# Kernel optimization log

Measured on AMD Instinct MI355X. Metric: run time of the kernel, lower is better.

Reference implementation:

```python
import jax, jax.numpy as jnp
import numpy as np

TEMP = 0.1
LAM = 1.0
NORM_EPS = 1e-12   # torch F.normalize eps
COS_EPS = 1e-8     # torch F.cosine_similarity eps


def l2norm(x, axis):
    n = jnp.sqrt(jnp.sum(x * x, axis=axis, keepdims=True))
    return x / jnp.maximum(n, NORM_EPS)


def cos_sim(a, b, axis):
    na = jnp.sqrt(jnp.sum(a * a, axis=axis))
    nb = jnp.sqrt(jnp.sum(b * b, axis=axis))
    return jnp.sum(a * b, axis=axis) / jnp.maximum(na * nb, COS_EPS)


def setup_inputs() -> dict:
    key = jax.random.key(0)
    k1, k2, k3, k4, k5 = jax.random.split(key, 5)
    B, C, H, W = 32, 256, 32, 32
    return {
        "q_b": jax.random.normal(k1, (B, C, H, W), dtype=jnp.float32),
        "k_b": jax.random.normal(k2, (B, C, H, W), dtype=jnp.float32),
        "q_grid": jax.random.normal(k3, (B, C, H, W), dtype=jnp.float32),
        "k_grid": jax.random.normal(k4, (B, C, H, W), dtype=jnp.float32),
        "labels": jax.random.randint(k5, (B,), 0, 10, dtype=jnp.int64),
    }


def densecl(q_b, k_b, q_grid, k_grid, labels):
    B, C, H, W = q_b.shape
    S = H * W
    q_b = l2norm(q_b, axis=1)
    k_b = l2norm(k_b, axis=1)
    q_grid = l2norm(q_grid, axis=1)
    k_grid = l2norm(k_grid, axis=1)

    q_b_flat = q_b.reshape(B, C, S)
    k_b_flat = k_b.reshape(B, C, S)
    # spatial correspondence: [B, S, S]
    sim = jnp.einsum('bci,bcj->bij', q_b_flat, k_b_flat)
    max_sim_idx = jnp.argmax(sim, axis=-1)  # [B, S]

    Cg = q_grid.shape[1]
    q_grid_flat = q_grid.reshape(B, Cg, S)
    k_grid_flat = k_grid.reshape(B, Cg, S)
    idx = jnp.broadcast_to(max_sim_idx[:, None, :], (B, Cg, S))
    k_matched = jnp.take_along_axis(k_grid_flat, idx, axis=2)
    pos_sim = cos_sim(q_grid_flat, k_matched, axis=1) / TEMP  # [B, S]

    # random negative from a different-label sample (use_prototypes=False path)
    key = jax.random.key(42)
    u = jax.random.uniform(key, (B, B))
    mask = labels[:, None] != labels[None, :]
    neg_idx = jnp.argmax(jnp.where(mask, u, -1.0), axis=1)  # [B]
    neg_k = k_grid_flat[neg_idx]  # [B, Cg, S]
    neg_sim = cos_sim(q_grid_flat, neg_k, axis=1) / TEMP  # [B, S]

    loss = -jnp.log(jnp.exp(pos_sim) / (jnp.exp(pos_sim) + jnp.exp(neg_sim) + 1e-6))
    return jnp.mean(loss)


def reference(q_b, k_b, q_grid, k_grid, labels):
    return densecl(q_b, k_b, q_grid, k_grid, labels) * LAM
```

## Files before the change

kernel.cpp:

```cpp
#include <hip/hip_runtime.h>
#include <hip/hip_bf16.h>
#include <math.h>
#include <stdint.h>

#define BB 32
#define CC 256
#define SS 1024

typedef __attribute__((ext_vector_type(8))) short short8v;
typedef __attribute__((ext_vector_type(4))) float f32x4;

#define ASYNC16(g, l)                                                        \
  __builtin_amdgcn_global_load_lds(                                          \
      (const __attribute__((address_space(1))) void*)(g),                    \
      (__attribute__((address_space(3))) void*)(l), 16, 0, 0)

__device__ __forceinline__ unsigned short bf16_rne(float f) {
  unsigned int u = __float_as_uint(f);
  unsigned int r = (u + 0x7fffu + ((u >> 16) & 1u)) >> 16;
  return (unsigned short)r;
}

__global__ __launch_bounds__(256, 4) void transnorm_kernel(
    const float* __restrict__ srcA, const float* __restrict__ srcB,
    unsigned short* __restrict__ dstA, unsigned short* __restrict__ dstB,
    float* __restrict__ invA, float* __restrict__ invB) {
  const int bid = blockIdx.x;
  const int which = bid >> 10;
  const int sub = bid & 1023;
  const int b = sub >> 5;
  const int s0 = (sub & 31) * 32;

  const float* src = which ? srcB : srcA;
  unsigned short* dst = which ? dstB : dstA;
  float* inv = which ? invB : invA;

  __shared__ float st[256][33];
  __shared__ float part[8][33];

  const int tid = threadIdx.x;
  const int s_l = tid & 31, c_off = tid >> 5;

  const float* sp = src + (size_t)b * CC * SS + s0 + s_l;
  float ssq = 0.f;
#pragma unroll 8
  for (int p = 0; p < 32; ++p) {
    int c = p * 8 + c_off;
    float x = sp[(size_t)c << 10];
    ssq = fmaf(x, x, ssq);
    st[c][s_l] = x;
  }
  part[c_off][s_l] = ssq;
  __syncthreads();

  const int chunk = tid >> 3, rb8 = tid & 7;
  unsigned short* dp = dst + ((size_t)b * SS + s0) * CC;
#pragma unroll
  for (int r0 = 0; r0 < 32; r0 += 8) {
    int r = r0 + rb8;
    unsigned short u[8];
#pragma unroll
    for (int uu = 0; uu < 8; ++uu) u[uu] = bf16_rne(st[chunk * 8 + uu][r]);
    uint4 pk;
    pk.x = (unsigned)u[0] | ((unsigned)u[1] << 16);
    pk.y = (unsigned)u[2] | ((unsigned)u[3] << 16);
    pk.z = (unsigned)u[4] | ((unsigned)u[5] << 16);
    pk.w = (unsigned)u[6] | ((unsigned)u[7] << 16);
    *(uint4*)(dp + (size_t)r * CC + chunk * 8) = pk;
  }
  if (tid < 32) {
    float s = 0.f;
#pragma unroll
    for (int k = 0; k < 8; ++k) s += part[k][tid];
    inv[b * SS + s0 + tid] = 1.0f / fmaxf(sqrtf(s), 1e-12f);
  }
}

__global__ __launch_bounds__(256, 3) void simargmax_mfma(
    const unsigned short* __restrict__ qt, const unsigned short* __restrict__ kt,
    const float* __restrict__ invk, unsigned long long* __restrict__ best) {
  const int bid = blockIdx.x;
  const int b = bid >> 6, it = (bid >> 3) & 7, jt = bid & 7;
  const int t = threadIdx.x, w = t >> 6, l = t & 63;

  __shared__ unsigned short sa[128 * 64];
  __shared__ unsigned short sb[128 * 64];
  __shared__ unsigned long long cand2[128][2];
  __shared__ float sinvk[128];

  if (t < 128) sinvk[t] = invk[b * SS + jt * 128 + t];

  const unsigned short* aG = qt + ((size_t)b * SS + it * 128) * CC;
  const unsigned short* bG = kt + ((size_t)b * SS + jt * 128) * CC;

  f32x4 acc[4][4];
#pragma unroll
  for (int mt = 0; mt < 4; ++mt)
#pragma unroll
    for (int nt = 0; nt < 4; ++nt) acc[mt][nt] = (f32x4){0.f, 0.f, 0.f, 0.f};

  const int r8 = l >> 3, p = l & 7;
  const int q4 = l >> 4, m16 = l & 15;
  const int wi = (w >> 1) * 64, wj = (w & 1) * 64;

  for (int ch = 0; ch < 4; ++ch) {
    __syncthreads();
#pragma unroll
    for (int v = 0; v < 4; ++v) {
      int r = v * 32 + w * 8 + r8;
      int clog = p ^ (r & 7);
      ASYNC16(aG + (size_t)r * CC + ch * 64 + clog * 8, &sa[(v * 32 + w * 8) * 64]);
      ASYNC16(bG + (size_t)r * CC + ch * 64 + clog * 8, &sb[(v * 32 + w * 8) * 64]);
    }
    __syncthreads();
#pragma unroll
    for (int kk = 0; kk < 2; ++kk) {
      short8v af[4], bf[4];
#pragma unroll
      for (int mt = 0; mt < 4; ++mt) {
        int i = wi + mt * 16 + m16;
        int cp = (kk * 4 + q4) ^ (i & 7);
        af[mt] = *(const short8v*)&sa[i * 64 + cp * 8];
        int j = wj + mt * 16 + m16;
        int cq = (kk * 4 + q4) ^ (j & 7);
        bf[mt] = *(const short8v*)&sb[j * 64 + cq * 8];
      }
#pragma unroll
      for (int mt = 0; mt < 4; ++mt)
#pragma unroll
        for (int nt = 0; nt < 4; ++nt)
          acc[mt][nt] = __builtin_amdgcn_mfma_f32_16x16x32_bf16(
              af[mt], bf[nt], acc[mt][nt], 0, 0, 0);
    }
  }

  float siv[4];
#pragma unroll
  for (int nt = 0; nt < 4; ++nt) siv[nt] = sinvk[wj + nt * 16 + m16];

  unsigned long long bp[4][4];
#pragma unroll
  for (int mt = 0; mt < 4; ++mt) {
#pragma unroll
    for (int e = 0; e < 4; ++e) {
      unsigned long long mx = 0ull;
#pragma unroll
      for (int nt = 0; nt < 4; ++nt) {
        float v = acc[mt][nt][e] * siv[nt];
        unsigned int u = __float_as_uint(v);
        u = (u & 0x80000000u) ? ~u : (u | 0x80000000u);
        int col = jt * 128 + wj + nt * 16 + m16;
        unsigned long long pk =
            ((unsigned long long)u << 32) | (unsigned)(1023 - col);
        mx = (pk > mx) ? pk : mx;
      }
      bp[mt][e] = mx;
    }
  }
#pragma unroll
  for (int d = 1; d < 16; d <<= 1) {
#pragma unroll
    for (int mt = 0; mt < 4; ++mt)
#pragma unroll
      for (int e = 0; e < 4; ++e) {
        unsigned long long o = __shfl_xor(bp[mt][e], d, 64);
        if (o > bp[mt][e]) bp[mt][e] = o;
      }
  }
  if (m16 == 0) {
#pragma unroll
    for (int mt = 0; mt < 4; ++mt)
#pragma unroll
      for (int e = 0; e < 4; ++e)
        cand2[wi + mt * 16 + q4 * 4 + e][w & 1] = bp[mt][e];
  }
  __syncthreads();
  if (t < 128) {
    unsigned long long m0 = cand2[t][0], m1 = cand2[t][1];
    atomicMax(&best[b * SS + it * 128 + t], m0 > m1 ? m0 : m1);
  }
}

__device__ __forceinline__ void tf_round(uint32_t& x0, uint32_t& x1, int r) {
  x0 += x1;
  x1 = (x1 << r) | (x1 >> (32 - r));
  x1 ^= x0;
}

__global__ void negidx_kernel(const int* __restrict__ labels, int* __restrict__ negidx) {
  __shared__ float u[1024];
  int t = threadIdx.x;
  uint32_t x0 = (uint32_t)t;
  uint32_t x1 = (uint32_t)(t + 512);
  const uint32_t ks0 = 0u, ks1 = 42u, ks2 = 0x1BD11BDAu ^ 0u ^ 42u;
  x0 += ks0; x1 += ks1;
  tf_round(x0, x1, 13); tf_round(x0, x1, 15); tf_round(x0, x1, 26); tf_round(x0, x1, 6);
  x0 += ks1; x1 += ks2 + 1u;
  tf_round(x0, x1, 17); tf_round(x0, x1, 29); tf_round(x0, x1, 16); tf_round(x0, x1, 24);
  x0 += ks2; x1 += ks0 + 2u;
  tf_round(x0, x1, 13); tf_round(x0, x1, 15); tf_round(x0, x1, 26); tf_round(x0, x1, 6);
  x0 += ks0; x1 += ks1 + 3u;
  tf_round(x0, x1, 17); tf_round(x0, x1, 29); tf_round(x0, x1, 16); tf_round(x0, x1, 24);
  x0 += ks1; x1 += ks2 + 4u;
  tf_round(x0, x1, 13); tf_round(x0, x1, 15); tf_round(x0, x1, 26); tf_round(x0, x1, 6);
  x0 += ks2; x1 += ks0 + 5u;
  u[t]       = __uint_as_float((x0 >> 9) | 0x3f800000u) - 1.0f;
  u[t + 512] = __uint_as_float((x1 >> 9) | 0x3f800000u) - 1.0f;
  __syncthreads();
  if (t < BB) {
    int lb = labels[t];
    float bestv = -1.0f;
    int bj = 0;
    for (int j = 0; j < BB; ++j) {
      float v = (labels[j] != lb) ? u[t * BB + j] : -1.0f;
      if (v > bestv) { bestv = v; bj = j; }
    }
    negidx[t] = bj;
  }
}

__global__ __launch_bounds__(256) void loss_fused_kernel(
    const float* __restrict__ qg, const unsigned short* __restrict__ kgt,
    const float* __restrict__ invkg, const unsigned long long* __restrict__ best,
    const int* __restrict__ negidx, float* __restrict__ out) {
  const int tid = threadIdx.x;
  const int s_l = tid & 31, g = tid >> 5;
  const int P0 = blockIdx.x * 32;
  const int b = P0 >> 10;
  const int s = (P0 & (SS - 1)) + s_l;
  const int idx = b * SS + s;
  const int js = 1023 - (int)(best[idx] & 0xffffffffu);
  const int nb = negidx[b];

  const float* qcol = qg + ((size_t)b * CC + g * 32) * SS + s;
  const unsigned short* kp = kgt + ((size_t)b * SS + js) * CC + g * 32;
  const unsigned short* kn = kgt + ((size_t)nb * SS + s) * CC + g * 32;

  float dp = 0.f, dn = 0.f, sq = 0.f;
#pragma unroll
  for (int uu = 0; uu < 4; ++uu) {
    uint4 up = *(const uint4*)(kp + uu * 8);
    uint4 un = *(const uint4*)(kn + uu * 8);
    float q[8];
#pragma unroll
    for (int j = 0; j < 8; ++j) {
      q[j] = qcol[(size_t)(uu * 8 + j) << 10];
      sq = fmaf(q[j], q[j], sq);
    }
    float pv[8], nv[8];
    pv[0] = __uint_as_float(up.x << 16); pv[1] = __uint_as_float(up.x & 0xffff0000u);
    pv[2] = __uint_as_float(up.y << 16); pv[3] = __uint_as_float(up.y & 0xffff0000u);
    pv[4] = __uint_as_float(up.z << 16); pv[5] = __uint_as_float(up.z & 0xffff0000u);
    pv[6] = __uint_as_float(up.w << 16); pv[7] = __uint_as_float(up.w & 0xffff0000u);
    nv[0] = __uint_as_float(un.x << 16); nv[1] = __uint_as_float(un.x & 0xffff0000u);
    nv[2] = __uint_as_float(un.y << 16); nv[3] = __uint_as_float(un.y & 0xffff0000u);
    nv[4] = __uint_as_float(un.z << 16); nv[5] = __uint_as_float(un.z & 0xffff0000u);
    nv[6] = __uint_as_float(un.w << 16); nv[7] = __uint_as_float(un.w & 0xffff0000u);
#pragma unroll
    for (int j = 0; j < 8; ++j) {
      dp = fmaf(q[j], pv[j], dp);
      dn = fmaf(q[j], nv[j], dn);
    }
  }

  __shared__ float rdp[8][33], rdn[8][33], rsq[8][33];
  rdp[g][s_l] = dp;
  rdn[g][s_l] = dn;
  rsq[g][s_l] = sq;
  __syncthreads();
  if (tid < 32) {
    float DP = 0.f, DN = 0.f, SQ = 0.f;
#pragma unroll
    for (int k = 0; k < 8; ++k) {
      DP += rdp[k][tid];
      DN += rdn[k][tid];
      SQ += rsq[k][tid];
    }
    int s2 = (P0 & (SS - 1)) + tid;
    int idx2 = b * SS + s2;
    int js2 = 1023 - (int)(best[idx2] & 0xffffffffu);
    float iq = 1.0f / fmaxf(sqrtf(SQ), 1e-12f);
    float pvv = DP * iq * invkg[b * SS + js2] * 10.0f;
    float nvv = DN * iq * invkg[nb * SS + s2] * 10.0f;
    float elem = logf(expf(pvv) + expf(nvv) + 1e-6f) - pvv;
#pragma unroll
    for (int o = 16; o > 0; o >>= 1) elem += __shfl_down(elem, o, 32);
    if (tid == 0) atomicAdd(out, elem * (1.0f / (BB * SS)));
  }
}

__global__ __launch_bounds__(256) void norms_kernel(
    const float* __restrict__ qb, const float* __restrict__ kb,
    const float* __restrict__ qg, const float* __restrict__ kg,
    float* __restrict__ inv) {
  int t = blockIdx.x * 256 + threadIdx.x;
  int which = t >> 15;
  int bs = t & (BB * SS - 1);
  const float* src = (which == 0) ? qb : (which == 1) ? kb : (which == 2) ? qg : kg;
  int b = bs >> 10;
  int s = bs & (SS - 1);
  const float* p = src + (size_t)b * CC * SS + s;
  float ss = 0.f;
#pragma unroll 8
  for (int c = 0; c < CC; ++c) {
    float x = p[(size_t)c * SS];
    ss = fmaf(x, x, ss);
  }
  float n = fmaxf(sqrtf(ss), 1e-12f);
  inv[t] = 1.0f / n;
}

#define TI 64
#define TJ 128
#define KC 32

__global__ __launch_bounds__(256) void simargmax_kernel(
    const float* __restrict__ qb, const float* __restrict__ kb,
    const float* __restrict__ invq, const float* __restrict__ invk,
    int* __restrict__ amax) {
  const int b = blockIdx.x >> 4;
  const int i0 = (blockIdx.x & 15) * TI;
  const int t = threadIdx.x;
  const int ti = t >> 4;
  const int tj = t & 15;

  __shared__ float aQ[KC][TI];
  __shared__ float bK[KC][TJ];
  __shared__ float redv[TI][16];
  __shared__ int redj[TI][16];

  const float* qbase = qb + (size_t)b * CC * SS + i0;
  const float* kbase = kb + (size_t)b * CC * SS;
  const float* ivq = invq + b * SS + i0;
  const float* ivk = invk + b * SS;

  float best_v = -3.4e38f;
  int best_j = 0;

  for (int j0 = 0; j0 < SS; j0 += TJ) {
    float acc[4][8];
#pragma unroll
    for (int r = 0; r < 4; ++r)
#pragma unroll
      for (int rr = 0; rr < 8; ++rr) acc[r][rr] = 0.f;

    for (int c0 = 0; c0 < CC; c0 += KC) {
      __syncthreads();
#pragma unroll
      for (int v = 0; v < 2; ++v) {
        int f = t + v * 256;
        int cl = f >> 4;
        int sl = (f & 15) << 2;
        float4 qa = *(const float4*)(qbase + (size_t)(c0 + cl) * SS + sl);
        float4 iv = *(const float4*)(ivq + sl);
        aQ[cl][sl + 0] = qa.x * iv.x;
        aQ[cl][sl + 1] = qa.y * iv.y;
        aQ[cl][sl + 2] = qa.z * iv.z;
        aQ[cl][sl + 3] = qa.w * iv.w;
      }
#pragma unroll
      for (int v = 0; v < 4; ++v) {
        int f = t + v * 256;
        int cl = f >> 5;
        int sl = (f & 31) << 2;
        float4 ka = *(const float4*)(kbase + (size_t)(c0 + cl) * SS + j0 + sl);
        float4 ik = *(const float4*)(ivk + j0 + sl);
        bK[cl][sl + 0] = ka.x * ik.x;
        bK[cl][sl + 1] = ka.y * ik.y;
        bK[cl][sl + 2] = ka.z * ik.z;
        bK[cl][sl + 3] = ka.w * ik.w;
      }
      __syncthreads();
#pragma unroll
      for (int kc = 0; kc < KC; ++kc) {
        float4 a0 = *(const float4*)&aQ[kc][ti * 4];
        float4 b0 = *(const float4*)&bK[kc][tj * 8];
        float4 b1 = *(const float4*)&bK[kc][tj * 8 + 4];
        float av[4] = {a0.x, a0.y, a0.z, a0.w};
        float bv[8] = {b0.x, b0.y, b0.z, b0.w, b1.x, b1.y, b1.z, b1.w};
#pragma unroll
        for (int r = 0; r < 4; ++r)
#pragma unroll
          for (int rr = 0; rr < 8; ++rr)
            acc[r][rr] = fmaf(av[r], bv[rr], acc[r][rr]);
      }
    }
    __syncthreads();
#pragma unroll
    for (int r = 0; r < 4; ++r) {
      float v = acc[r][0];
      int jb = j0 + tj * 8;
#pragma unroll
      for (int rr = 1; rr < 8; ++rr) {
        if (acc[r][rr] > v) { v = acc[r][rr]; jb = j0 + tj * 8 + rr; }
      }
      redv[ti * 4 + r][tj] = v;
      redj[ti * 4 + r][tj] = jb;
    }
    __syncthreads();
    if (t < TI) {
#pragma unroll
      for (int ww = 0; ww < 16; ++ww) {
        float v = redv[t][ww];
        if (v > best_v) { best_v = v; best_j = redj[t][ww]; }
      }
    }
  }
  if (t < TI) amax[b * SS + i0 + t] = best_j;
}

__global__ __launch_bounds__(256) void loss_kernel(
    const float* __restrict__ qg, const float* __restrict__ kg,
    const float* __restrict__ invq, const float* __restrict__ invk,
    const int* __restrict__ amax, const int* __restrict__ negidx,
    float* __restrict__ out) {
  int t = blockIdx.x * 256 + threadIdx.x;
  int b = t >> 10;
  int s = t & (SS - 1);
  int js = amax[t];
  int nb = negidx[b];
  const float* qcol = qg + (size_t)b * CC * SS + s;
  const float* kpcol = kg + (size_t)b * CC * SS + js;
  const float* kncol = kg + (size_t)nb * CC * SS + s;
  float dp = 0.f, dn = 0.f;
#pragma unroll 8
  for (int c = 0; c < CC; ++c) {
    float q = qcol[(size_t)c * SS];
    dp = fmaf(q, kpcol[(size_t)c * SS], dp);
    dn = fmaf(q, kncol[(size_t)c * SS], dn);
  }
  float iq = invq[t];
  float pv = dp * iq * invk[b * SS + js] * 10.0f;
  float nv = dn * iq * invk[nb * SS + s] * 10.0f;
  float elem = logf(expf(pv) + expf(nv) + 1e-6f) - pv;

  __shared__ float red[256];
  red[threadIdx.x] = elem;
  __syncthreads();
  for (int o = 128; o > 0; o >>= 1) {
    if (threadIdx.x < o) red[threadIdx.x] += red[threadIdx.x + o];
    __syncthreads();
  }
  if (threadIdx.x == 0) atomicAdd(out, red[0] * (1.0f / (BB * SS)));
}

extern "C" void kernel_launch(void* const* d_in, const int* in_sizes, int n_in,
                              void* d_out, int out_size, void* d_ws, size_t ws_size,
                              hipStream_t stream) {
  const float* qb = (const float*)d_in[0];
  const float* kb = (const float*)d_in[1];
  const float* qg = (const float*)d_in[2];
  const float* kg = (const float*)d_in[3];
  const int* labels = (const int*)d_in[4];

  char* ws = (char*)d_ws;
  float* invqb = (float*)ws;
  float* invkb = (float*)(ws + 128 * 1024);
  float* invkg = (float*)(ws + 256 * 1024);
  unsigned long long* best = (unsigned long long*)(ws + 384 * 1024);
  int* negidx = (int*)(ws + 640 * 1024);
  unsigned short* qt = (unsigned short*)(ws + (1 << 20));
  unsigned short* kt = (unsigned short*)(ws + (17 << 20));
  unsigned short* kgt = qt;

  const size_t need = (size_t)33 * 1024 * 1024;
  const bool fast = ws_size >= need;

  hipMemsetAsync(d_out, 0, sizeof(float), stream);

  if (fast) {
    hipMemsetAsync(best, 0, BB * SS * sizeof(unsigned long long), stream);
    negidx_kernel<<<1, 512, 0, stream>>>(labels, negidx);
    transnorm_kernel<<<2048, 256, 0, stream>>>(qb, kb, qt, kt, invqb, invkb);
    simargmax_mfma<<<2048, 256, 0, stream>>>(qt, kt, invkb, best);
    transnorm_kernel<<<1024, 256, 0, stream>>>(kg, kg, kgt, kgt, invkg, invkg);
    loss_fused_kernel<<<1024, 256, 0, stream>>>(qg, kgt, invkg, best, negidx,
                                                (float*)d_out);
  } else {
    float* inv = (float*)ws;
    int* amax = (int*)(ws + 512 * 1024);
    int* negidx2 = (int*)(ws + 640 * 1024);
    norms_kernel<<<(4 * BB * SS) / 256, 256, 0, stream>>>(qb, kb, qg, kg, inv);
    simargmax_kernel<<<BB * (SS / TI), 256, 0, stream>>>(
        qb, kb, inv + 0 * BB * SS, inv + 1 * BB * SS, amax);
    negidx_kernel<<<1, 512, 0, stream>>>(labels, negidx2);
    loss_kernel<<<(BB * SS) / 256, 256, 0, stream>>>(
        qg, kg, inv + 2 * BB * SS, inv + 3 * BB * SS, amax, negidx2,
        (float*)d_out);
  }
}
```

Before: 219.0 us.

## Merge prep launches into one transpose-normalize kernel with zeroing and negidx

Folds the two memsets, the negidx kernel and both transnorm launches into a single 3077-block launch. Extra blocks zero the argmax buffer and compute the negative indices, and the k_grid transpose gets its own workspace region so it can run alongside q_b/k_b instead of after the sim-argmax. This removes several launch and serialization gaps. In exchange it needs more workspace (49 MB instead of 33 MB), and if the workspace is too small the slower fallback path runs.

After: 207.1 us. 5.4% less time.

```diff
diff --git a/kernel.cpp b/kernel.cpp
--- a/kernel.cpp
+++ b/kernel.cpp
@@ -21,175 +21,13 @@
   return (unsigned short)r;
 }
 
-__global__ __launch_bounds__(256, 4) void transnorm_kernel(
-    const float* __restrict__ srcA, const float* __restrict__ srcB,
-    unsigned short* __restrict__ dstA, unsigned short* __restrict__ dstB,
-    float* __restrict__ invA, float* __restrict__ invB) {
-  const int bid = blockIdx.x;
-  const int which = bid >> 10;
-  const int sub = bid & 1023;
-  const int b = sub >> 5;
-  const int s0 = (sub & 31) * 32;
-
-  const float* src = which ? srcB : srcA;
-  unsigned short* dst = which ? dstB : dstA;
-  float* inv = which ? invB : invA;
-
-  __shared__ float st[256][33];
-  __shared__ float part[8][33];
-
-  const int tid = threadIdx.x;
-  const int s_l = tid & 31, c_off = tid >> 5;
-
-  const float* sp = src + (size_t)b * CC * SS + s0 + s_l;
-  float ssq = 0.f;
-#pragma unroll 8
-  for (int p = 0; p < 32; ++p) {
-    int c = p * 8 + c_off;
-    float x = sp[(size_t)c << 10];
-    ssq = fmaf(x, x, ssq);
-    st[c][s_l] = x;
-  }
-  part[c_off][s_l] = ssq;
-  __syncthreads();
-
-  const int chunk = tid >> 3, rb8 = tid & 7;
-  unsigned short* dp = dst + ((size_t)b * SS + s0) * CC;
-#pragma unroll
-  for (int r0 = 0; r0 < 32; r0 += 8) {
-    int r = r0 + rb8;
-    unsigned short u[8];
-#pragma unroll
-    for (int uu = 0; uu < 8; ++uu) u[uu] = bf16_rne(st[chunk * 8 + uu][r]);
-    uint4 pk;
-    pk.x = (unsigned)u[0] | ((unsigned)u[1] << 16);
-    pk.y = (unsigned)u[2] | ((unsigned)u[3] << 16);
-    pk.z = (unsigned)u[4] | ((unsigned)u[5] << 16);
-    pk.w = (unsigned)u[6] | ((unsigned)u[7] << 16);
-    *(uint4*)(dp + (size_t)r * CC + chunk * 8) = pk;
-  }
-  if (tid < 32) {
-    float s = 0.f;
-#pragma unroll
-    for (int k = 0; k < 8; ++k) s += part[k][tid];
-    inv[b * SS + s0 + tid] = 1.0f / fmaxf(sqrtf(s), 1e-12f);
-  }
-}
-
-__global__ __launch_bounds__(256, 3) void simargmax_mfma(
-    const unsigned short* __restrict__ qt, const unsigned short* __restrict__ kt,
-    const float* __restrict__ invk, unsigned long long* __restrict__ best) {
-  const int bid = blockIdx.x;
-  const int b = bid >> 6, it = (bid >> 3) & 7, jt = bid & 7;
-  const int t = threadIdx.x, w = t >> 6, l = t & 63;
-
-  __shared__ unsigned short sa[128 * 64];
-  __shared__ unsigned short sb[128 * 64];
-  __shared__ unsigned long long cand2[128][2];
-  __shared__ float sinvk[128];
-
-  if (t < 128) sinvk[t] = invk[b * SS + jt * 128 + t];
-
-  const unsigned short* aG = qt + ((size_t)b * SS + it * 128) * CC;
-  const unsigned short* bG = kt + ((size_t)b * SS + jt * 128) * CC;
-
-  f32x4 acc[4][4];
-#pragma unroll
-  for (int mt = 0; mt < 4; ++mt)
-#pragma unroll
-    for (int nt = 0; nt < 4; ++nt) acc[mt][nt] = (f32x4){0.f, 0.f, 0.f, 0.f};
-
-  const int r8 = l >> 3, p = l & 7;
-  const int q4 = l >> 4, m16 = l & 15;
-  const int wi = (w >> 1) * 64, wj = (w & 1) * 64;
-
-  for (int ch = 0; ch < 4; ++ch) {
-    __syncthreads();
-#pragma unroll
-    for (int v = 0; v < 4; ++v) {
-      int r = v * 32 + w * 8 + r8;
-      int clog = p ^ (r & 7);
-      ASYNC16(aG + (size_t)r * CC + ch * 64 + clog * 8, &sa[(v * 32 + w * 8) * 64]);
-      ASYNC16(bG + (size_t)r * CC + ch * 64 + clog * 8, &sb[(v * 32 + w * 8) * 64]);
-    }
-    __syncthreads();
-#pragma unroll
-    for (int kk = 0; kk < 2; ++kk) {
-      short8v af[4], bf[4];
-#pragma unroll
-      for (int mt = 0; mt < 4; ++mt) {
-        int i = wi + mt * 16 + m16;
-        int cp = (kk * 4 + q4) ^ (i & 7);
-        af[mt] = *(const short8v*)&sa[i * 64 + cp * 8];
-        int j = wj + mt * 16 + m16;
-        int cq = (kk * 4 + q4) ^ (j & 7);
-        bf[mt] = *(const short8v*)&sb[j * 64 + cq * 8];
-      }
-#pragma unroll
-      for (int mt = 0; mt < 4; ++mt)
-#pragma unroll
-        for (int nt = 0; nt < 4; ++nt)
-          acc[mt][nt] = __builtin_amdgcn_mfma_f32_16x16x32_bf16(
-              af[mt], bf[nt], acc[mt][nt], 0, 0, 0);
-    }
-  }
-
-  float siv[4];
-#pragma unroll
-  for (int nt = 0; nt < 4; ++nt) siv[nt] = sinvk[wj + nt * 16 + m16];
-
-  unsigned long long bp[4][4];
-#pragma unroll
-  for (int mt = 0; mt < 4; ++mt) {
-#pragma unroll
-    for (int e = 0; e < 4; ++e) {
-      unsigned long long mx = 0ull;
-#pragma unroll
-      for (int nt = 0; nt < 4; ++nt) {
-        float v = acc[mt][nt][e] * siv[nt];
-        unsigned int u = __float_as_uint(v);
-        u = (u & 0x80000000u) ? ~u : (u | 0x80000000u);
-        int col = jt * 128 + wj + nt * 16 + m16;
-        unsigned long long pk =
-            ((unsigned long long)u << 32) | (unsigned)(1023 - col);
-        mx = (pk > mx) ? pk : mx;
-      }
-      bp[mt][e] = mx;
-    }
-  }
-#pragma unroll
-  for (int d = 1; d < 16; d <<= 1) {
-#pragma unroll
-    for (int mt = 0; mt < 4; ++mt)
-#pragma unroll
-      for (int e = 0; e < 4; ++e) {
-        unsigned long long o = __shfl_xor(bp[mt][e], d, 64);
-        if (o > bp[mt][e]) bp[mt][e] = o;
-      }
-  }
-  if (m16 == 0) {
-#pragma unroll
-    for (int mt = 0; mt < 4; ++mt)
-#pragma unroll
-      for (int e = 0; e < 4; ++e)
-        cand2[wi + mt * 16 + q4 * 4 + e][w & 1] = bp[mt][e];
-  }
-  __syncthreads();
-  if (t < 128) {
-    unsigned long long m0 = cand2[t][0], m1 = cand2[t][1];
-    atomicMax(&best[b * SS + it * 128 + t], m0 > m1 ? m0 : m1);
-  }
-}
-
 __device__ __forceinline__ void tf_round(uint32_t& x0, uint32_t& x1, int r) {
   x0 += x1;
   x1 = (x1 << r) | (x1 >> (32 - r));
   x1 ^= x0;
 }
 
-__global__ void negidx_kernel(const int* __restrict__ labels, int* __restrict__ negidx) {
-  __shared__ float u[1024];
-  int t = threadIdx.x;
+__device__ __forceinline__ void tf_gen(int t, float* u) {
   uint32_t x0 = (uint32_t)t;
   uint32_t x1 = (uint32_t)(t + 512);
   const uint32_t ks0 = 0u, ks1 = 42u, ks2 = 0x1BD11BDAu ^ 0u ^ 42u;
@@ -206,6 +44,202 @@
   x0 += ks2; x1 += ks0 + 5u;
   u[t]       = __uint_as_float((x0 >> 9) | 0x3f800000u) - 1.0f;
   u[t + 512] = __uint_as_float((x1 >> 9) | 0x3f800000u) - 1.0f;
+}
+
+__global__ __launch_bounds__(256, 4) void transnorm_kernel(
+    const float* __restrict__ qb, const float* __restrict__ kb,
+    const float* __restrict__ kg, unsigned short* __restrict__ qt,
+    unsigned short* __restrict__ kt, unsigned short* __restrict__ kgt,
+    float* __restrict__ invqb, float* __restrict__ invkb,
+    float* __restrict__ invkg, const int* __restrict__ labels,
+    int* __restrict__ negidx, unsigned long long* __restrict__ best,
+    float* __restrict__ out) {
+  const int bid = blockIdx.x;
+  const int tid = threadIdx.x;
+
+  __shared__ float st[256][33];
+  __shared__ float part[8][33];
+
+  if (bid >= 3072) {
+    if (bid == 3072) {
+      float* u = &st[0][0];
+      tf_gen(tid, u);
+      tf_gen(tid + 256, u);
+      if (tid == 0) *out = 0.f;
+      __syncthreads();
+      if (tid < BB) {
+        int lb = labels[tid];
+        float bestv = -1.0f;
+        int bj = 0;
+        for (int j = 0; j < BB; ++j) {
+          float v = (labels[j] != lb) ? u[tid * BB + j] : -1.0f;
+          if (v > bestv) { bestv = v; bj = j; }
+        }
+        negidx[tid] = bj;
+      }
+    } else {
+      unsigned long long* bp = best + (size_t)(bid - 3073) * 8192 + tid;
+#pragma unroll
+      for (int i = 0; i < 32; ++i) bp[(size_t)i * 256] = 0ull;
+    }
+    return;
+  }
+
+  const int which = bid >> 10;
+  const int sub = bid & 1023;
+  const int b = sub >> 5;
+  const int s0 = (sub & 31) * 32;
+
+  const float* src = (which == 0) ? qb : (which == 1) ? kb : kg;
+  unsigned short* dst = (which == 0) ? qt : (which == 1) ? kt : kgt;
+  float* inv = (which == 0) ? invqb : (which == 1) ? invkb : invkg;
+
+  const int s_l = tid & 31, c_off = tid >> 5;
+
+  const float* sp = src + (size_t)b * CC * SS + s0 + s_l;
+  float ssq = 0.f;
+#pragma unroll 8
+  for (int p = 0; p < 32; ++p) {
+    int c = p * 8 + c_off;
+    float x = sp[(size_t)c << 10];
+    ssq = fmaf(x, x, ssq);
+    st[c][s_l] = x;
+  }
+  part[c_off][s_l] = ssq;
+  __syncthreads();
+
+  const int chunk = tid >> 3, rb8 = tid & 7;
+  unsigned short* dp = dst + ((size_t)b * SS + s0) * CC;
+#pragma unroll
+  for (int r0 = 0; r0 < 32; r0 += 8) {
+    int r = r0 + rb8;
+    unsigned short u[8];
+#pragma unroll
+    for (int uu = 0; uu < 8; ++uu) u[uu] = bf16_rne(st[chunk * 8 + uu][r]);
+    uint4 pk;
+    pk.x = (unsigned)u[0] | ((unsigned)u[1] << 16);
+    pk.y = (unsigned)u[2] | ((unsigned)u[3] << 16);
+    pk.z = (unsigned)u[4] | ((unsigned)u[5] << 16);
+    pk.w = (unsigned)u[6] | ((unsigned)u[7] << 16);
+    *(uint4*)(dp + (size_t)r * CC + chunk * 8) = pk;
+  }
+  if (tid < 32) {
+    float s = 0.f;
+#pragma unroll
+    for (int k = 0; k < 8; ++k) s += part[k][tid];
+    inv[b * SS + s0 + tid] = 1.0f / fmaxf(sqrtf(s), 1e-12f);
+  }
+}
+
+__global__ __launch_bounds__(256, 3) void simargmax_mfma(
+    const unsigned short* __restrict__ qt, const unsigned short* __restrict__ kt,
+    const float* __restrict__ invk, unsigned long long* __restrict__ best) {
+  const int bid = blockIdx.x;
+  const int b = bid >> 6, it = (bid >> 3) & 7, jt = bid & 7;
+  const int t = threadIdx.x, w = t >> 6, l = t & 63;
+
+  __shared__ unsigned short sa[128 * 64];
+  __shared__ unsigned short sb[128 * 64];
+  __shared__ unsigned long long cand2[128][2];
+  __shared__ float sinvk[128];
+
+  if (t < 128) sinvk[t] = invk[b * SS + jt * 128 + t];
+
+  const unsigned short* aG = qt + ((size_t)b * SS + it * 128) * CC;
+  const unsigned short* bG = kt + ((size_t)b * SS + jt * 128) * CC;
+
+  f32x4 acc[4][4];
+#pragma unroll
+  for (int mt = 0; mt < 4; ++mt)
+#pragma unroll
+    for (int nt = 0; nt < 4; ++nt) acc[mt][nt] = (f32x4){0.f, 0.f, 0.f, 0.f};
+
+  const int r8 = l >> 3, p = l & 7;
+  const int q4 = l >> 4, m16 = l & 15;
+  const int wi = (w >> 1) * 64, wj = (w & 1) * 64;
+
+  for (int ch = 0; ch < 4; ++ch) {
+    __syncthreads();
+#pragma unroll
+    for (int v = 0; v < 4; ++v) {
+      int r = v * 32 + w * 8 + r8;
+      int clog = p ^ (r & 7);
+      ASYNC16(aG + (size_t)r * CC + ch * 64 + clog * 8, &sa[(v * 32 + w * 8) * 64]);
+      ASYNC16(bG + (size_t)r * CC + ch * 64 + clog * 8, &sb[(v * 32 + w * 8) * 64]);
+    }
+    __syncthreads();
+#pragma unroll
+    for (int kk = 0; kk < 2; ++kk) {
+      short8v af[4], bf[4];
+#pragma unroll
+      for (int mt = 0; mt < 4; ++mt) {
+        int i = wi + mt * 16 + m16;
+        int cp = (kk * 4 + q4) ^ (i & 7);
+        af[mt] = *(const short8v*)&sa[i * 64 + cp * 8];
+        int j = wj + mt * 16 + m16;
+        int cq = (kk * 4 + q4) ^ (j & 7);
+        bf[mt] = *(const short8v*)&sb[j * 64 + cq * 8];
+      }
+#pragma unroll
+      for (int mt = 0; mt < 4; ++mt)
+#pragma unroll
+        for (int nt = 0; nt < 4; ++nt)
+          acc[mt][nt] = __builtin_amdgcn_mfma_f32_16x16x32_bf16(
+              af[mt], bf[nt], acc[mt][nt], 0, 0, 0);
+    }
+  }
+
+  float siv[4];
+#pragma unroll
+  for (int nt = 0; nt < 4; ++nt) siv[nt] = sinvk[wj + nt * 16 + m16];
+
+  unsigned long long bp[4][4];
+#pragma unroll
+  for (int mt = 0; mt < 4; ++mt) {
+#pragma unroll
+    for (int e = 0; e < 4; ++e) {
+      unsigned long long mx = 0ull;
+#pragma unroll
+      for (int nt = 0; nt < 4; ++nt) {
+        float v = acc[mt][nt][e] * siv[nt];
+        unsigned int u = __float_as_uint(v);
+        u = (u & 0x80000000u) ? ~u : (u | 0x80000000u);
+        int col = jt * 128 + wj + nt * 16 + m16;
+        unsigned long long pk =
+            ((unsigned long long)u << 32) | (unsigned)(1023 - col);
+        mx = (pk > mx) ? pk : mx;
+      }
+      bp[mt][e] = mx;
+    }
+  }
+#pragma unroll
+  for (int d = 1; d < 16; d <<= 1) {
+#pragma unroll
+    for (int mt = 0; mt < 4; ++mt)
+#pragma unroll
+      for (int e = 0; e < 4; ++e) {
+        unsigned long long o = __shfl_xor(bp[mt][e], d, 64);
+        if (o > bp[mt][e]) bp[mt][e] = o;
+      }
+  }
+  if (m16 == 0) {
+#pragma unroll
+    for (int mt = 0; mt < 4; ++mt)
+#pragma unroll
+      for (int e = 0; e < 4; ++e)
+        cand2[wi + mt * 16 + q4 * 4 + e][w & 1] = bp[mt][e];
+  }
+  __syncthreads();
+  if (t < 128) {
+    unsigned long long m0 = cand2[t][0], m1 = cand2[t][1];
+    atomicMax(&best[b * SS + it * 128 + t], m0 > m1 ? m0 : m1);
+  }
+}
+
+__global__ void negidx_kernel(const int* __restrict__ labels, int* __restrict__ negidx) {
+  __shared__ float u[1024];
+  int t = threadIdx.x;
+  tf_gen(t, u);
   __syncthreads();
   if (t < BB) {
     int lb = labels[t];
@@ -461,22 +495,20 @@
   int* negidx = (int*)(ws + 640 * 1024);
   unsigned short* qt = (unsigned short*)(ws + (1 << 20));
   unsigned short* kt = (unsigned short*)(ws + (17 << 20));
-  unsigned short* kgt = qt;
-
-  const size_t need = (size_t)33 * 1024 * 1024;
+  unsigned short* kgt = (unsigned short*)(ws + (33 << 20));
+
+  const size_t need = (size_t)49 * 1024 * 1024;
   const bool fast = ws_size >= need;
 
-  hipMemsetAsync(d_out, 0, sizeof(float), stream);
-
   if (fast) {
-    hipMemsetAsync(best, 0, BB * SS * sizeof(unsigned long long), stream);
-    negidx_kernel<<<1, 512, 0, stream>>>(labels, negidx);
-    transnorm_kernel<<<2048, 256, 0, stream>>>(qb, kb, qt, kt, invqb, invkb);
+    transnorm_kernel<<<3077, 256, 0, stream>>>(qb, kb, kg, qt, kt, kgt, invqb,
+                                               invkb, invkg, labels, negidx,
+                                               best, (float*)d_out);
     simargmax_mfma<<<2048, 256, 0, stream>>>(qt, kt, invkb, best);
-    transnorm_kernel<<<1024, 256, 0, stream>>>(kg, kg, kgt, kgt, invkg, invkg);
     loss_fused_kernel<<<1024, 256, 0, stream>>>(qg, kgt, invkg, best, negidx,
                                                 (float*)d_out);
   } else {
+    hipMemsetAsync(d_out, 0, sizeof(float), stream);
     float* inv = (float*)ws;
     int* amax = (int*)(ws + 512 * 1024);
     int* negidx2 = (int*)(ws + 640 * 1024);
```
